# Performance work log

Measured on AMD Instinct MI355X. Metric: run time of the kernel, lower is better.

The kernel has to match this reference:

```python
import jax, jax.numpy as jnp
import numpy as np

B, L, D, R = 16, 256, 1024, 128

def setup_inputs() -> dict:
    key = jax.random.key(0)
    k1, k2 = jax.random.split(key)
    batch = jax.random.normal(k1, (B, L, D), dtype=jnp.float32)
    # proj initialized uniform(-0.05, 0.05) in the original
    proj = jax.random.uniform(k2, (D, R), dtype=jnp.float32, minval=-0.05, maxval=0.05)
    return {"batch": batch, "proj": proj}

def reference(batch, proj):
    # [B, L, R] projected embeddings
    t = jnp.matmul(batch, proj)
    # all-pairs squared L2 distances: sum_r (t[b,i,r] - t[b,j,r])^2 -> [B, L, L]
    diffs = t[:, :, None, :] - t[:, None, :, :]  # [B, L, L, R]
    squared_distances = jnp.sum(diffs * diffs, axis=-1)
    return squared_distances
```

## Files before the change

### kernel.cpp

```cpp
#include <hip/hip_runtime.h>
#include <stdint.h>

#define B_ 16
#define L_ 256
#define D_ 1024
#define R_ 128
#define M_ (B_*L_)

typedef short short8 __attribute__((ext_vector_type(8)));
typedef float f32x4 __attribute__((ext_vector_type(4)));

__device__ __forceinline__ unsigned short f2bf(float f) {
  union { float f; unsigned int u; } v; v.f = f;
  unsigned int r = v.u + 0x7FFFu + ((v.u >> 16) & 1u);
  return (unsigned short)(r >> 16);
}
__device__ __forceinline__ float bf2f(unsigned short s) {
  union { unsigned int u; float f; } v; v.u = ((unsigned int)s) << 16;
  return v.f;
}
__device__ __forceinline__ void gload_lds16(const void* g, void* l) {
  __builtin_amdgcn_global_load_lds(
      (const __attribute__((address_space(1))) unsigned int*)g,
      (__attribute__((address_space(3))) unsigned int*)l, 16, 0, 0);
}

__global__ __launch_bounds__(256) void k0_transpose_cast(
    const float* __restrict__ P, unsigned short* __restrict__ PbT) {
  int id = blockIdx.x * 256 + threadIdx.x;
  int n  = id & 127;
  int kq = id >> 7;
  union { unsigned short s[4]; uint2 v; } u;
#pragma unroll
  for (int j = 0; j < 4; ++j) u.s[j] = f2bf(P[(kq * 4 + j) * R_ + n]);
  *reinterpret_cast<uint2*>(&PbT[(size_t)n * D_ + kq * 4]) = u.v;
}

__global__ __launch_bounds__(256) void k1_gemm(
    const float* __restrict__ X, const unsigned short* __restrict__ PbT,
    unsigned short* __restrict__ Tb) {
  __shared__ unsigned short sX[2][16 * 128];
  __shared__ unsigned short sP[2][64 * 128];

  const int tid  = threadIdx.x;
  const int lane = tid & 63;
  const int w    = tid >> 6;
  const int lb   = (blockIdx.x & 7) * 64 + (blockIdx.x >> 3);
  const int m0   = (lb >> 1) * 16;
  const int nb0  = (lb & 1) * 64;

  f32x4 acc;
  acc[0] = 0.f; acc[1] = 0.f; acc[2] = 0.f; acc[3] = 0.f;

  float4 xs[2][2];

  auto loadX = [&](float4* slot, int kt) {
#pragma unroll
    for (int i = 0; i < 2; ++i) {
      int c = tid + 256 * i;
      int row = c >> 5, kq = (c & 31) * 4;
      slot[i] = *reinterpret_cast<const float4*>(&X[(size_t)(m0 + row) * D_ + kt * 128 + kq]);
    }
  };
  auto writeX = [&](int buf, const float4* slot) {
#pragma unroll
    for (int i = 0; i < 2; ++i) {
      int c = tid + 256 * i;
      int row = c >> 5, kq = (c & 31) * 4;
      uint2 p;
      p.x = (unsigned int)f2bf(slot[i].x) | ((unsigned int)f2bf(slot[i].y) << 16);
      p.y = (unsigned int)f2bf(slot[i].z) | ((unsigned int)f2bf(slot[i].w) << 16);
      int byte_in_row = (kq * 2) ^ ((row & 7) << 4);
      *reinterpret_cast<uint2*>(reinterpret_cast<char*>(&sX[buf][0]) + row * 256 + byte_in_row) = p;
    }
  };
  auto issueP = [&](int buf, int kt) {
    const int k0 = kt * 128;
#pragma unroll
    for (int i = 0; i < 4; ++i) {
      int c = tid + 256 * i;
      int row = c >> 4, ch = c & 15;
      gload_lds16(&PbT[(size_t)(nb0 + row) * D_ + k0 + ((ch ^ (row & 7)) * 8)],
                  reinterpret_cast<char*>(&sP[buf][0]) + c * 16);
    }
  };
  auto compute = [&](int buf) {
    const char* xb = reinterpret_cast<const char*>(&sX[buf][0]);
    const char* pb = reinterpret_cast<const char*>(&sP[buf][0]);
#pragma unroll
    for (int s = 0; s < 4; ++s) {
      int koffb = s * 64 + ((lane >> 4) << 4);
      int ar = lane & 15;
      short8 a = *reinterpret_cast<const short8*>(xb + ar * 256 + (koffb ^ ((ar & 7) << 4)));
      int br = w * 16 + (lane & 15);
      short8 b = *reinterpret_cast<const short8*>(pb + br * 256 + (koffb ^ ((br & 7) << 4)));
      acc = __builtin_amdgcn_mfma_f32_16x16x32_bf16(a, b, acc, 0, 0, 0);
    }
  };

  loadX(xs[0], 0);
  issueP(0, 0);
  loadX(xs[1], 1);
  writeX(0, xs[0]);

#pragma unroll
  for (int kt = 0; kt < 8; ++kt) {
    const int buf = kt & 1;
    if (kt == 7) asm volatile("s_waitcnt vmcnt(0) lgkmcnt(0)" ::: "memory");
    else         asm volatile("s_waitcnt vmcnt(2) lgkmcnt(0)" ::: "memory");
    __builtin_amdgcn_sched_barrier(0);
    __builtin_amdgcn_s_barrier();
    compute(buf);
    if (kt < 7) issueP(buf ^ 1, kt + 1);
    if (kt < 6) loadX(xs[kt & 1], kt + 2);
    if (kt < 7) writeX(buf ^ 1, xs[(kt + 1) & 1]);
  }

  const int col = lane & 15;
#pragma unroll
  for (int q = 0; q < 4; ++q) {
    int row = ((lane >> 4) << 2) + q;
    Tb[(size_t)(m0 + row) * R_ + nb0 + w * 16 + col] = f2bf(acc[q]);
  }
}

__global__ __launch_bounds__(256) void k2_gram(
    const unsigned short* __restrict__ Tb, float* __restrict__ Out) {
  __shared__ unsigned short sI[16 * 128];
  __shared__ unsigned short sJ[64 * 128];
  __shared__ float nI[16], nJ[64];

  const int tid  = threadIdx.x;
  const int lane = tid & 63;
  const int w    = tid >> 6;
  const int blk  = blockIdx.x;
  const int b    = blk >> 6;
  const int it   = (blk >> 2) & 15;
  const int jq   = blk & 3;

  {
    int row = tid >> 4, ch = tid & 15;
    gload_lds16(&Tb[(size_t)(b * L_ + it * 16 + row) * R_ + ((ch ^ (row & 7)) * 8)],
                reinterpret_cast<char*>(sI) + tid * 16);
  }
#pragma unroll
  for (int i = 0; i < 4; ++i) {
    int c = tid + 256 * i;
    int row = c >> 4, ch = c & 15;
    gload_lds16(&Tb[(size_t)(b * L_ + jq * 64 + row) * R_ + ((ch ^ (row & 7)) * 8)],
                reinterpret_cast<char*>(sJ) + c * 16);
  }
  __syncthreads();

  if (tid < 160) {
    int row = tid >> 1, h = tid & 1;
    const char* base = (row < 16) ? reinterpret_cast<const char*>(sI)
                                  : reinterpret_cast<const char*>(sJ);
    int r = (row < 16) ? row : row - 16;
    float s = 0.f;
#pragma unroll
    for (int j = 0; j < 8; ++j) {
      short8 v = *reinterpret_cast<const short8*>(base + r * 256 + ((h * 128 + j * 16) ^ ((r & 7) << 4)));
#pragma unroll
      for (int e = 0; e < 8; ++e) { float f = bf2f((unsigned short)v[e]); s += f * f; }
    }
    s += __shfl_xor(s, 1);
    if (h == 0) { if (row < 16) nI[row] = s; else nJ[row - 16] = s; }
  }

  f32x4 acc;
  acc[0] = 0.f; acc[1] = 0.f; acc[2] = 0.f; acc[3] = 0.f;
  const char* ib = reinterpret_cast<const char*>(sI);
  const char* jb = reinterpret_cast<const char*>(sJ);
#pragma unroll
  for (int s = 0; s < 4; ++s) {
    int koffb = s * 64 + ((lane >> 4) << 4);
    int ar = lane & 15;
    short8 a = *reinterpret_cast<const short8*>(ib + ar * 256 + (koffb ^ ((ar & 7) << 4)));
    int br = w * 16 + (lane & 15);
    short8 bv = *reinterpret_cast<const short8*>(jb + br * 256 + (koffb ^ ((br & 7) << 4)));
    acc = __builtin_amdgcn_mfma_f32_16x16x32_bf16(a, bv, acc, 0, 0, 0);
  }
  __syncthreads();

  const int col = lane & 15;
  const int jj = w * 16 + col;
  const float nj = nJ[jj];
#pragma unroll
  for (int q = 0; q < 4; ++q) {
    int ir = ((lane >> 4) << 2) + q;
    float v = nI[ir] + nj - 2.0f * acc[q];
    Out[(size_t)(b * L_ + it * 16 + ir) * L_ + jq * 64 + jj] = fmaxf(v, 0.0f);
  }
}

extern "C" void kernel_launch(void* const* d_in, const int* in_sizes, int n_in,
                              void* d_out, int out_size, void* d_ws, size_t ws_size,
                              hipStream_t stream) {
  const float* X = (const float*)d_in[0];
  const float* P = (const float*)d_in[1];
  float* Out = (float*)d_out;
  char* ws = (char*)d_ws;
  unsigned short* PbT = (unsigned short*)ws;
  unsigned short* Tb  = (unsigned short*)(ws + (size_t)R_ * D_ * 2);

  k0_transpose_cast<<<128, 256, 0, stream>>>(P, PbT);
  k1_gemm<<<M_ / 16 * 2, 256, 0, stream>>>(X, PbT, Tb);
  k2_gram<<<B_ * 16 * 4, 256, 0, stream>>>(Tb, Out);
}
```

Measured before the change: 20.73 us.

## Fuse projection transpose-cast into GEMM, loading fp32 P directly

Removes the separate kernel that converted the projection matrix to transposed bf16, and has the GEMM load fp32 P tiles into registers, pack pairs with v_cvt_pk_bf16_f32 and write them transposed and swizzled into LDS. This drops one kernel launch and the round trip through workspace. In exchange every GEMM block re-reads and re-converts fp32 P, which doubles P load bytes and adds register pressure and LDS store work. The software pipeline is also reordered so register-staged loads and LDS writes replace the async global-to-LDS copy.

Measured after the change: 27.42 us. 32.2% more time.

```diff
diff --git a/kernel.cpp b/kernel.cpp
--- a/kernel.cpp
+++ b/kernel.cpp
@@ -25,19 +25,8 @@
       (__attribute__((address_space(3))) unsigned int*)l, 16, 0, 0);
 }
 
-__global__ __launch_bounds__(256) void k0_transpose_cast(
-    const float* __restrict__ P, unsigned short* __restrict__ PbT) {
-  int id = blockIdx.x * 256 + threadIdx.x;
-  int n  = id & 127;
-  int kq = id >> 7;
-  union { unsigned short s[4]; uint2 v; } u;
-#pragma unroll
-  for (int j = 0; j < 4; ++j) u.s[j] = f2bf(P[(kq * 4 + j) * R_ + n]);
-  *reinterpret_cast<uint2*>(&PbT[(size_t)n * D_ + kq * 4]) = u.v;
-}
-
 __global__ __launch_bounds__(256) void k1_gemm(
-    const float* __restrict__ X, const unsigned short* __restrict__ PbT,
+    const float* __restrict__ X, const float* __restrict__ P,
     unsigned short* __restrict__ Tb) {
   __shared__ unsigned short sX[2][16 * 128];
   __shared__ unsigned short sP[2][64 * 128];
@@ -53,6 +42,7 @@
   acc[0] = 0.f; acc[1] = 0.f; acc[2] = 0.f; acc[3] = 0.f;
 
   float4 xs[2][2];
+  float4 ps[2][8];
 
   auto loadX = [&](float4* slot, int kt) {
 #pragma unroll
@@ -74,14 +64,35 @@
       *reinterpret_cast<uint2*>(reinterpret_cast<char*>(&sX[buf][0]) + row * 256 + byte_in_row) = p;
     }
   };
-  auto issueP = [&](int buf, int kt) {
+  auto loadP = [&](float4* slot, int kt) {
     const int k0 = kt * 128;
 #pragma unroll
     for (int i = 0; i < 4; ++i) {
       int c = tid + 256 * i;
-      int row = c >> 4, ch = c & 15;
-      gload_lds16(&PbT[(size_t)(nb0 + row) * D_ + k0 + ((ch ^ (row & 7)) * 8)],
-                  reinterpret_cast<char*>(&sP[buf][0]) + c * 16);
+      int kp = ((c >> 8) << 4) | (c & 15);
+      int nq = (c >> 4) & 15;
+      const float* base = &P[(size_t)(k0 + 2 * kp) * R_ + nb0 + 4 * nq];
+      slot[2 * i]     = *reinterpret_cast<const float4*>(base);
+      slot[2 * i + 1] = *reinterpret_cast<const float4*>(base + R_);
+    }
+  };
+  auto writeP = [&](int buf, const float4* slot) {
+    char* spb = reinterpret_cast<char*>(&sP[buf][0]);
+#pragma unroll
+    for (int i = 0; i < 4; ++i) {
+      int c = tid + 256 * i;
+      int kp = ((c >> 8) << 4) | (c & 15);
+      int nq = (c >> 4) & 15;
+      const float* lo = reinterpret_cast<const float*>(&slot[2 * i]);
+      const float* hi = reinterpret_cast<const float*>(&slot[2 * i + 1]);
+#pragma unroll
+      for (int e = 0; e < 4; ++e) {
+        int row = 4 * nq + e;
+        unsigned int pk;
+        asm("v_cvt_pk_bf16_f32 %0, %1, %2" : "=v"(pk) : "v"(lo[e]), "v"(hi[e]));
+        int byte_in_row = (4 * kp) ^ ((row & 7) << 4);
+        *reinterpret_cast<unsigned int*>(spb + row * 256 + byte_in_row) = pk;
+      }
     }
   };
   auto compute = [&](int buf) {
@@ -98,22 +109,23 @@
     }
   };
 
+  loadP(ps[0], 0);
   loadX(xs[0], 0);
-  issueP(0, 0);
+  writeP(0, ps[0]);
+  writeX(0, xs[0]);
+  loadP(ps[1], 1);
   loadX(xs[1], 1);
-  writeX(0, xs[0]);
 
 #pragma unroll
   for (int kt = 0; kt < 8; ++kt) {
     const int buf = kt & 1;
-    if (kt == 7) asm volatile("s_waitcnt vmcnt(0) lgkmcnt(0)" ::: "memory");
-    else         asm volatile("s_waitcnt vmcnt(2) lgkmcnt(0)" ::: "memory");
+    asm volatile("s_waitcnt lgkmcnt(0)" ::: "memory");
     __builtin_amdgcn_sched_barrier(0);
     __builtin_amdgcn_s_barrier();
+    __builtin_amdgcn_sched_barrier(0);
     compute(buf);
-    if (kt < 7) issueP(buf ^ 1, kt + 1);
-    if (kt < 6) loadX(xs[kt & 1], kt + 2);
-    if (kt < 7) writeX(buf ^ 1, xs[(kt + 1) & 1]);
+    if (kt < 7) { writeP(buf ^ 1, ps[(kt + 1) & 1]); writeX(buf ^ 1, xs[(kt + 1) & 1]); }
+    if (kt < 6) { loadP(ps[kt & 1], kt + 2); loadX(xs[kt & 1], kt + 2); }
   }
 
   const int col = lane & 15;
@@ -201,10 +213,8 @@
   const float* P = (const float*)d_in[1];
   float* Out = (float*)d_out;
   char* ws = (char*)d_ws;
-  unsigned short* PbT = (unsigned short*)ws;
-  unsigned short* Tb  = (unsigned short*)(ws + (size_t)R_ * D_ * 2);
-
-  k0_transpose_cast<<<128, 256, 0, stream>>>(P, PbT);
-  k1_gemm<<<M_ / 16 * 2, 256, 0, stream>>>(X, PbT, Tb);
+  unsigned short* Tb = (unsigned short*)ws;
+
+  k1_gemm<<<M_ / 16 * 2, 256, 0, stream>>>(X, P, Tb);
   k2_gram<<<B_ * 16 * 4, 256, 0, stream>>>(Tb, Out);
 }
```
